# Kernel tuning notes

Hardware: AMD Instinct MI355X
Metric: run time of the kernel (lower is better)

## Reference

```python
import jax, jax.numpy as jnp
import numpy as np

B, L, D = 2, 2048, 2048
H, HKV, HD = 16, 4, 128
GROUPS = H // HKV


def _rope_tables(key):
    # standard RoPE cos/sin tables, shape (B, L, HD)
    inv_freq = 1.0 / (10000.0 ** (jnp.arange(0, HD, 2, dtype=jnp.float32) / HD))
    pos = jnp.arange(L, dtype=jnp.float32)
    freqs = pos[:, None] * inv_freq[None, :]          # (L, HD/2)
    emb = jnp.concatenate([freqs, freqs], axis=-1)    # (L, HD)
    cos = jnp.broadcast_to(jnp.cos(emb)[None], (B, L, HD))
    sin = jnp.broadcast_to(jnp.sin(emb)[None], (B, L, HD))
    return cos, sin


def setup_inputs() -> dict:
    key = jax.random.key(0)
    ks = jax.random.split(key, 5)
    x = jax.random.normal(ks[0], (B, L, D), dtype=jnp.float32)
    cos, sin = _rope_tables(ks[1])
    s = 1.0 / np.sqrt(D)
    Wq = jax.random.normal(ks[2], (D, D), dtype=jnp.float32) * s
    bq = jnp.zeros((D,), dtype=jnp.float32)
    Wkv = jax.random.normal(ks[3], (2 * HKV * HD, D), dtype=jnp.float32) * s
    bkv = jnp.zeros((2 * HKV * HD,), dtype=jnp.float32)
    Wo = jax.random.normal(ks[4], (D, D), dtype=jnp.float32) * s
    bo = jnp.zeros((D,), dtype=jnp.float32)
    return {"x": x, "cos": cos, "sin": sin, "Wq": Wq, "bq": bq,
            "Wkv": Wkv, "bkv": bkv, "Wo": Wo, "bo": bo}


def _rotate_half(t):
    t1, t2 = jnp.split(t, 2, axis=-1)
    return jnp.concatenate([-t2, t1], axis=-1)


def reference(x, cos, sin, Wq, bq, Wkv, bkv, Wo, bo):
    b, l, d = x.shape
    # QKV projections
    q = (x @ Wq.T + bq).reshape(b, l, H, HD)
    kv = (x @ Wkv.T + bkv).reshape(b, l, 2, HKV, HD)
    k, v = kv[:, :, 0], kv[:, :, 1]
    # RoPE (unsqueeze over head dim, layout B,L,H,D)
    c = cos[:, :, None, :]
    s = sin[:, :, None, :]
    q = q * c + _rotate_half(q) * s
    k = k * c + _rotate_half(k) * s
    # GQA: expand kv heads to query heads
    k = jnp.repeat(k, GROUPS, axis=2)
    v = jnp.repeat(v, GROUPS, axis=2)
    # causal attention (flash_attn_func equivalent math)
    scores = jnp.einsum("blhd,bmhd->bhlm", q, k) / jnp.sqrt(jnp.float32(HD))
    mask = jnp.tril(jnp.ones((l, l), dtype=bool))
    scores = jnp.where(mask[None, None], scores, jnp.finfo(scores.dtype).min)
    attn = jax.nn.softmax(scores, axis=-1)
    out = jnp.einsum("bhlm,bmhd->blhd", attn, v).reshape(b, l, H * HD)
    return out @ Wo.T + bo
```

## Files before the change

kernel.cpp:

```cpp
#include <hip/hip_runtime.h>
#include <hip/hip_bf16.h>
#include <cstddef>

constexpr int B = 2, L = 2048, D = 2048;
constexpr int H = 16, HKV = 4, HD = 128;
constexpr int GROUPS = H / HKV;
constexpr int KVD = 2 * HKV * HD;
constexpr int M_ROWS = B * L;
constexpr int QKVW = D + KVD;

typedef __attribute__((ext_vector_type(8))) short short8;
typedef __attribute__((ext_vector_type(4))) short s16x4;
typedef __attribute__((ext_vector_type(4))) float f32x4;

__device__ __forceinline__ short f2bf(float f) {
    union { float f; unsigned u; } v; v.f = f;
    unsigned r = v.u + 0x7FFFu + ((v.u >> 16) & 1u);
    return (short)(r >> 16);
}

__device__ __forceinline__ float fast_exp2(float x) {
#if __has_builtin(__builtin_amdgcn_exp2f)
    return __builtin_amdgcn_exp2f(x);
#else
    return exp2f(x);
#endif
}

__device__ __forceinline__ int invp(int pos) {
    const int b16 = pos >> 4, j = pos & 15;
    return ((b16 >> 1) << 4) + j + ((b16 & 1) << 6);
}

typedef __attribute__((address_space(1))) const void cg_void;
typedef __attribute__((address_space(3))) void lds_void;
__device__ __forceinline__ void gl_lds16(const void* g, void* l) {
    __builtin_amdgcn_global_load_lds((cg_void*)g, (lds_void*)l, 16, 0, 0);
}

__global__ __launch_bounds__(256) void cast_all(
    const float* __restrict__ x, const float* __restrict__ Wq,
    const float* __restrict__ Wkv, const float* __restrict__ Wo,
    const float* __restrict__ bq, const float* __restrict__ bkv,
    short* __restrict__ xb, short* __restrict__ wqkvb, short* __restrict__ wob,
    float* __restrict__ bqkv)
{
    constexpr int n_x   = M_ROWS * D / 4;
    constexpr int n_wq  = D * D / 4;
    constexpr int n_wkv = KVD * D / 4;
    constexpr int n_wo  = D * D / 4;
    constexpr int n_w   = n_x + n_wq + n_wkv + n_wo;
    constexpr int RPW   = D / 4;
    int i = blockIdx.x * 256 + threadIdx.x;
    if (i >= n_w) {
        const int j = i - n_w;
        float4 o;
#pragma unroll
        for (int e = 0; e < 4; ++e) {
            const int idx = j * 4 + e;
            float v;
            if (idx < D)                 v = bq[((idx >> 7) << 7) + invp(idx & 127)];
            else if (idx < D + HKV * HD) v = bkv[(((idx - D) >> 7) << 7) + invp((idx - D) & 127)];
            else                         v = bkv[idx - D];
            (&o.x)[e] = v;
        }
        ((float4*)bqkv)[j] = o;
        return;
    }
    const float* src; short* dst; int isrc;
    if (i < n_x) {
        src = x; dst = xb; isrc = i;
    } else if (i < n_x + n_wq) {
        i -= n_x; src = Wq; dst = wqkvb;
        const int fi = i / RPW, col = i % RPW;
        const int head = fi >> 7, pos = fi & 127;
        isrc = ((head << 7) + invp(pos)) * RPW + col;
    } else if (i < n_x + n_wq + n_wkv) {
        i -= n_x + n_wq; src = Wkv; dst = wqkvb + (size_t)D * D;
        const int fi = i / RPW, col = i % RPW;
        if (fi < HKV * HD) {
            isrc = (((fi >> 7) << 7) + invp(fi & 127)) * RPW + col;
        } else {
            isrc = i;
        }
    } else {
        i -= n_x + n_wq + n_wkv; src = Wo; dst = wob; isrc = i;
    }
    const float4 f = ((const float4*)src)[isrc];
    s16x4 s;
    s[0] = f2bf(f.x); s[1] = f2bf(f.y); s[2] = f2bf(f.z); s[3] = f2bf(f.w);
    ((s16x4*)dst)[i] = s;
}

template<int MODE>
__global__ __launch_bounds__(512, 2) void gemm256(
    const short* __restrict__ Ag, const short* __restrict__ Wg,
    const float* __restrict__ bias, float* __restrict__ C,
    const float* __restrict__ cosp, const float* __restrict__ sinp,
    short* __restrict__ qout, short* __restrict__ kout, short* __restrict__ vtout,
    int M, int N, int K)
{
    __shared__ __align__(1024) char smem[131072];

    const int tid = threadIdx.x;
    const int w = tid >> 6, lane = tid & 63;
    const int quad = lane >> 4, n16 = lane & 15;
    const int wr = w >> 2, wc = w & 3;

    const int nbx = gridDim.x;
    const int nwg = nbx * gridDim.y;
    int wg = blockIdx.y * nbx + blockIdx.x;
    wg = (wg & 7) * (nwg >> 3) + (wg >> 3);
    const int bm = (wg / nbx) << 8;
    const int bn = (wg % nbx) << 8;

    const int nkt = K >> 6;

    const int sbo = n16 * 64 + ((quad * 16) ^ ((n16 & 8) << 2));

    const int srow = lane >> 2;
    const int scol = ((lane & 3) * 8) ^ (((lane >> 5) & 1) << 4);

    f32x4 acc[8][4];
#pragma unroll
    for (int i = 0; i < 8; ++i)
#pragma unroll
        for (int j = 0; j < 4; ++j)
#pragma unroll
            for (int r = 0; r < 4; ++r) acc[i][j][r] = 0.f;

    short8 afr[4][2], bfr[4][2];

#define STAGE_A(k0, cb, h)                                                     \
    { _Pragma("unroll") for (int j = 0; j < 2; ++j) {                          \
        const int s  = w + j * 8;                                              \
        const int u  = s >> 1;                                                 \
        const int rg = ((u >> 2) << 3) + ((h) << 2) + (u & 3);                 \
        const int gr = bm + (rg << 4) + srow;                                  \
        const int gc = (k0) + ((s & 1) << 5) + scol;                           \
        gl_lds16(Ag + (size_t)gr * K + gc,                                     \
                 smem + (cb) * 32768 + (h) * 16384 + (s << 10)); } }

#define STAGE_B(k0, cb, h)                                                     \
    { _Pragma("unroll") for (int j = 0; j < 2; ++j) {                          \
        const int s  = w + j * 8;                                              \
        const int u  = s >> 1;                                                 \
        const int rg = ((u >> 1) << 2) + ((h) << 1) + (u & 1);                 \
        const int gr = bn + (rg << 4) + srow;                                  \
        const int gc = (k0) + ((s & 1) << 5) + scol;                           \
        gl_lds16(Wg + (size_t)gr * K + gc,                                     \
                 smem + 65536 + (cb) * 32768 + (h) * 16384 + (s << 10)); } }

#define PHASE(CB, MH, RDB, STAGE_STMT, WAIT_STMT)                              \
    {                                                                          \
        if (RDB) {                                                             \
            _Pragma("unroll") for (int nj = 0; nj < 4; ++nj)                   \
            _Pragma("unroll") for (int kk = 0; kk < 2; ++kk)                   \
                bfr[nj][kk] = *(const short8*)(smem + 65536 + (CB) * 32768 +   \
                    (nj >> 1) * 16384 +                                        \
                    ((((wc * 2 + (nj & 1)) * 2) + kk) << 10) + sbo);           \
        }                                                                      \
        _Pragma("unroll") for (int mi2 = 0; mi2 < 4; ++mi2)                    \
        _Pragma("unroll") for (int kk = 0; kk < 2; ++kk)                       \
            afr[mi2][kk] = *(const short8*)(smem + (CB) * 32768 +              \
                (MH) * 16384 + ((((wr * 4 + mi2) * 2) + kk) << 10) + sbo);     \
        STAGE_STMT;                                                            \
        WAIT_STMT;                                                             \
        __builtin_amdgcn_s_barrier();                                          \
        asm volatile("s_waitcnt lgkmcnt(0)" ::: "memory");                     \
        __builtin_amdgcn_sched_barrier(0);                                     \
        __builtin_amdgcn_s_setprio(1);                                         \
        _Pragma("unroll") for (int mi2 = 0; mi2 < 4; ++mi2)                    \
        _Pragma("unroll") for (int nj = 0; nj < 4; ++nj)                       \
        _Pragma("unroll") for (int kk = 0; kk < 2; ++kk)                       \
            acc[(MH) * 4 + mi2][nj] =                                          \
                __builtin_amdgcn_mfma_f32_16x16x32_bf16(                       \
                    afr[mi2][kk], bfr[nj][kk], acc[(MH) * 4 + mi2][nj],        \
                    0, 0, 0);                                                  \
        __builtin_amdgcn_s_setprio(0);                                         \
        asm volatile("" ::: "memory");                                         \
        __builtin_amdgcn_s_barrier();                                          \
    }

#define NOP_WAIT asm volatile("" ::: "memory")

    STAGE_A(0, 0, 0);
    STAGE_B(0, 0, 0);
    STAGE_A(0, 0, 1);
    STAGE_B(0, 0, 1);
    if (nkt > 1) {
        STAGE_A(64, 1, 0);
        STAGE_B(64, 1, 0);
        asm volatile("s_waitcnt vmcnt(4)" ::: "memory");
    } else {
        asm volatile("s_waitcnt vmcnt(0)" ::: "memory");
    }
    __builtin_amdgcn_s_barrier();

    for (int t = 0; t < nkt; t += 2) {
        const int k1 = (t + 1) << 6, k2 = (t + 2) << 6, k3 = (t + 3) << 6;
        const bool g2 = (t + 2) < nkt, g3 = (t + 3) < nkt;

        PHASE(0, 0, 1, { STAGE_A(k1, 1, 1); STAGE_B(k1, 1, 1); }, NOP_WAIT);
        PHASE(0, 1, 0, { if (g2) { STAGE_A(k2, 0, 0); STAGE_B(k2, 0, 0); } },
              { if (g2) asm volatile("s_waitcnt vmcnt(4)" ::: "memory");
                else    asm volatile("s_waitcnt vmcnt(0)" ::: "memory"); });

        PHASE(1, 0, 1, { if (g2) { STAGE_A(k2, 0, 1); STAGE_B(k2, 0, 1); } }, NOP_WAIT);
        PHASE(1, 1, 0, { if (g3) { STAGE_A(k3, 1, 0); STAGE_B(k3, 1, 0); } },
              { if (g3) asm volatile("s_waitcnt vmcnt(4)" ::: "memory");
                else    asm volatile("s_waitcnt vmcnt(0)" ::: "memory"); });
    }

#undef PHASE
#undef STAGE_A
#undef STAGE_B
#undef NOP_WAIT

    if (MODE == 0) {
#pragma unroll
        for (int mh = 0; mh < 2; ++mh)
#pragma unroll
            for (int mi2 = 0; mi2 < 4; ++mi2)
#pragma unroll
                for (int r = 0; r < 4; ++r) {
                    const int row = bm + wr * 128 + mh * 64 + mi2 * 16 + quad * 4 + r;
#pragma unroll
                    for (int nh = 0; nh < 2; ++nh)
#pragma unroll
                        for (int ni2 = 0; ni2 < 2; ++ni2) {
                            const int col = bn + wc * 64 + nh * 32 + ni2 * 16 + n16;
                            C[(size_t)row * N + col] =
                                acc[mh * 4 + mi2][nh * 2 + ni2][r] + bias[col];
                        }
                }
    } else {
        short* const T = (short*)smem;
        __syncthreads();
        if (bn < D + HKV * HD) {
#pragma unroll
            for (int mh = 0; mh < 2; ++mh)
#pragma unroll
                for (int mi2 = 0; mi2 < 4; ++mi2)
#pragma unroll
                    for (int r = 0; r < 4; ++r) {
                        const int rl = wr * 128 + mh * 64 + mi2 * 16 + quad * 4 + r;
                        const int row = bm + rl;
                        const float* csrow = cosp + (size_t)row * HD;
                        const float* snrow = sinp + (size_t)row * HD;
                        const int sw = ((rl >> 2) & 7) << 4;
#pragma unroll
                        for (int nh = 0; nh < 2; ++nh) {
                            const int cl = wc * 64 + nh * 32 + n16;
                            const int iif = (wc & 1) * 32 + nh * 16 + n16;
                            const float a  = acc[mh * 4 + mi2][nh * 2 + 0][r] + bias[bn + cl];
                            const float bb = acc[mh * 4 + mi2][nh * 2 + 1][r] + bias[bn + cl + 16];
                            const float olo = a * csrow[iif]       - bb * snrow[iif];
                            const float ohi = bb * csrow[iif + 64] + a * snrow[iif + 64];
                            *(short*)((char*)T + ((rl * 512 + cl * 2) ^ sw))        = f2bf(olo);
                            *(short*)((char*)T + ((rl * 512 + (cl + 16) * 2) ^ sw)) = f2bf(ohi);
                        }
                    }
            __syncthreads();
            const bool isK = (bn >= D);
#pragma unroll
            for (int it = 0; it < 16; ++it) {
                const int idx = it * 512 + tid;
                const int rl = idx >> 5, c8 = idx & 31;
                const short8 v = *(const short8*)((char*)T +
                    ((rl * 512 + c8 * 16) ^ (((rl >> 2) & 7) << 4)));
                const int row = bm + rl;
                if (!isK) {
                    *(short8*)&qout[(size_t)row * D + bn + c8 * 8] = v;
                } else {
                    const int ck = bn - D + c8 * 8;
                    const int hk = ck >> 7, dk = ck & 127;
                    const int b_ = row >> 11, l_ = row & (L - 1);
                    *(short8*)&kout[((size_t)(b_ * HKV + hk) * L + l_) * HD + dk] = v;
                }
            }
        } else {
#pragma unroll
            for (int mh = 0; mh < 2; ++mh)
#pragma unroll
                for (int mi2 = 0; mi2 < 4; ++mi2) {
                    const int l0 = wr * 128 + mh * 64 + mi2 * 16 + quad * 4;
#pragma unroll
                    for (int nh = 0; nh < 2; ++nh)
#pragma unroll
                        for (int ni2 = 0; ni2 < 2; ++ni2) {
                            const int cl = wc * 64 + nh * 32 + ni2 * 16 + n16;
                            const float bs = bias[bn + cl];
                            s16x4 sv;
#pragma unroll
                            for (int r = 0; r < 4; ++r)
                                sv[r] = f2bf(acc[mh * 4 + mi2][nh * 2 + ni2][r] + bs);
                            *(s16x4*)((char*)T + ((cl * 512 + l0 * 2) ^ ((cl & 7) << 4))) = sv;
                        }
                }
            __syncthreads();
#pragma unroll
            for (int it = 0; it < 16; ++it) {
                const int idx = it * 512 + tid;
                const int cvr = idx >> 5, l8 = idx & 31;
                const short8 v = *(const short8*)((char*)T +
                    ((cvr * 512 + l8 * 16) ^ ((cvr & 7) << 4)));
                const int cv = bn - (D + HKV * HD) + cvr;
                const int hv = cv >> 7, dv = cv & 127;
                const int b_ = bm >> 11;
                const int lg = (bm & (L - 1)) + l8 * 8;
                *(short8*)&vtout[((size_t)(b_ * HKV + hv) * HD + dv) * L + lg] = v;
            }
        }
    }
}

__global__ __launch_bounds__(512, 2) void gemm_out(
    const short* __restrict__ Ag, const short* __restrict__ Wg,
    const float* __restrict__ bias, float* __restrict__ C,
    int M, int N, int K)
{
    __shared__ __align__(1024) char smem[98304];

    const int tid = threadIdx.x;
    const int w = tid >> 6, lane = tid & 63;
    const int quad = lane >> 4, n16 = lane & 15;
    const int wr = w >> 2, wc = w & 3;

    const int nbx = gridDim.x;
    const int nwg = nbx * gridDim.y;
    int wg = blockIdx.y * nbx + blockIdx.x;
    wg = (wg & 7) * (nwg >> 3) + (wg >> 3);
    const int bm = (wg / nbx) << 7;
    const int bn = (wg % nbx) << 8;

    const int nkt = K >> 6;

    const int sbo = n16 * 64 + ((quad * 16) ^ ((n16 & 8) << 2));
    const int srow = lane >> 2;
    const int scol = ((lane & 3) * 8) ^ (((lane >> 5) & 1) << 4);

    f32x4 acc[4][4];
#pragma unroll
    for (int i = 0; i < 4; ++i)
#pragma unroll
        for (int j = 0; j < 4; ++j)
#pragma unroll
            for (int r = 0; r < 4; ++r) acc[i][j][r] = 0.f;

    short8 afr[4], bfr[4];

#define OSTAGE_A(k0, cb, kh)                                                   \
    { const int gr = bm + (w << 4) + srow;                                     \
      const int gc = (k0) + ((kh) << 5) + scol;                                \
      gl_lds16(Ag + (size_t)gr * K + gc,                                       \
               smem + (cb) * 16384 + (kh) * 8192 + (w << 10)); }

#define OSTAGE_B(k0, cb, kh)                                                   \
    { _Pragma("unroll") for (int j = 0; j < 2; ++j) {                          \
        const int s = w + j * 8;                                               \
        const int gr = bn + (s << 4) + srow;                                   \
        const int gc = (k0) + ((kh) << 5) + scol;                              \
        gl_lds16(Wg + (size_t)gr * K + gc,                                     \
                 smem + 32768 + (cb) * 32768 + (kh) * 16384 + (s << 10)); } }

#define OPHASE(CB, KH, STAGE_STMT, WAIT_STMT)                                  \
    {                                                                          \
        _Pragma("unroll") for (int mi = 0; mi < 4; ++mi)                       \
            afr[mi] = *(const short8*)(smem + (CB) * 16384 + (KH) * 8192 +     \
                ((wr * 4 + mi) << 10) + sbo);                                  \
        _Pragma("unroll") for (int nj = 0; nj < 4; ++nj)                       \
            bfr[nj] = *(const short8*)(smem + 32768 + (CB) * 32768 +           \
                (KH) * 16384 + ((wc * 4 + nj) << 10) + sbo);                   \
        STAGE_STMT;                                                            \
        WAIT_STMT;                                                             \
        __builtin_amdgcn_s_barrier();                                          \
        asm volatile("s_waitcnt lgkmcnt(0)" ::: "memory");                     \
        __builtin_amdgcn_sched_barrier(0);                                     \
        __builtin_amdgcn_s_setprio(1);                                         \
        _Pragma("unroll") for (int mi = 0; mi < 4; ++mi)                       \
        _Pragma("unroll") for (int nj = 0; nj < 4; ++nj)                       \
            acc[mi][nj] = __builtin_amdgcn_mfma_f32_16x16x32_bf16(             \
                afr[mi], bfr[nj], acc[mi][nj], 0, 0, 0);                       \
        __builtin_amdgcn_s_setprio(0);                                         \
        asm volatile("" ::: "memory");                                         \
        __builtin_amdgcn_s_barrier();                                          \
    }

#define ONOP asm volatile("" ::: "memory")

    OSTAGE_A(0, 0, 0);
    OSTAGE_B(0, 0, 0);
    OSTAGE_A(0, 0, 1);
    OSTAGE_B(0, 0, 1);
    if (nkt > 1) {
        OSTAGE_A(64, 1, 0);
        OSTAGE_B(64, 1, 0);
        asm volatile("s_waitcnt vmcnt(3)" ::: "memory");
    } else {
        asm volatile("s_waitcnt vmcnt(0)" ::: "memory");
    }
    __builtin_amdgcn_s_barrier();

    for (int t = 0; t < nkt; t += 2) {
        const int k1 = (t + 1) << 6, k2 = (t + 2) << 6, k3 = (t + 3) << 6;
        const bool g2 = (t + 2) < nkt, g3 = (t + 3) < nkt;

        OPHASE(0, 0, { OSTAGE_A(k1, 1, 1); OSTAGE_B(k1, 1, 1); }, ONOP);
        OPHASE(0, 1, { if (g2) { OSTAGE_A(k2, 0, 0); OSTAGE_B(k2, 0, 0); } },
               { if (g2) asm volatile("s_waitcnt vmcnt(3)" ::: "memory");
                 else    asm volatile("s_waitcnt vmcnt(0)" ::: "memory"); });

        OPHASE(1, 0, { if (g2) { OSTAGE_A(k2, 0, 1); OSTAGE_B(k2, 0, 1); } }, ONOP);
        OPHASE(1, 1, { if (g3) { OSTAGE_A(k3, 1, 0); OSTAGE_B(k3, 1, 0); } },
               { if (g3) asm volatile("s_waitcnt vmcnt(3)" ::: "memory");
                 else    asm volatile("s_waitcnt vmcnt(0)" ::: "memory"); });
    }

#undef OPHASE
#undef OSTAGE_A
#undef OSTAGE_B
#undef ONOP

#pragma unroll
    for (int mi = 0; mi < 4; ++mi)
#pragma unroll
        for (int r = 0; r < 4; ++r) {
            const int row = bm + wr * 64 + mi * 16 + quad * 4 + r;
#pragma unroll
            for (int nj = 0; nj < 4; ++nj) {
                const int col = bn + wc * 64 + nj * 16 + n16;
                C[(size_t)row * N + col] = acc[mi][nj][r] + bias[col];
            }
        }
}

__global__ __launch_bounds__(512) void attn_mfma4(
    const short* __restrict__ qb_, const short* __restrict__ kb_,
    const short* __restrict__ vtb_, short* __restrict__ ob)
{
    __shared__ __align__(16) char smem[86016];
    short* const KsB  = (short*)smem;
    short* const VtB  = (short*)(smem + 32768);
    short* const PbB  = (short*)(smem + 65536);
    float* const Rbuf = (float*)smem;

    const int hkv = blockIdx.y, b = blockIdx.z;
    const int tid = threadIdx.x;
    const int w = tid >> 6, lane = tid & 63;
    const int quad = lane >> 4, n16 = lane & 15;
    const int h   = hkv * GROUPS + (w & 3);
    const int kh  = (w >> 2) * 32;
    const int khg = (w >> 2) * 4;

    const size_t kbase  = (size_t)(b * HKV + hkv) * L * HD;
    const size_t vtbase = (size_t)(b * HKV + hkv) * HD * L;
    const float c1 = 0.12751845f;
    const float c0 = -28.853901f;

    short8 ones;
#pragma unroll
    for (int i = 0; i < 8; ++i) ones[i] = (short)0x3F80;

    const int kr = lane >> 4;
    const int kg_sw = lane & 15;
    const int vr = lane >> 3;
    const int vg_sw = lane & 7;

    short* const myPb = PbB + w * (2 * 16 * 40);

#pragma unroll 1
    for (int phase = 0; phase < 2; ++phase) {
        const int qidx = phase ? (63 - (int)blockIdx.x) : (int)blockIdx.x;
        const int qb0 = qidx * 32;
        const int ntiles = (qidx >> 1) + 1;

        short8 qf[2][4];
#pragma unroll
        for (int rt = 0; rt < 2; ++rt)
#pragma unroll
            for (int kk = 0; kk < 4; ++kk)
                qf[rt][kk] = *(const short8*)&qb_[
                    ((size_t)(b * L + qb0 + rt * 16 + n16)) * D + h * HD + kk * 32 + quad * 8];

        f32x4 oacc[2][8], lacc[2];
#pragma unroll
        for (int rt = 0; rt < 2; ++rt) {
#pragma unroll
            for (int r = 0; r < 4; ++r) lacc[rt][r] = 0.f;
#pragma unroll
            for (int nt = 0; nt < 8; ++nt)
#pragma unroll
                for (int r = 0; r < 4; ++r) oacc[rt][nt][r] = 0.f;
        }

        __syncthreads();

        {
            const short* kg = kb_ + kbase;
            const short* vg = vtb_ + vtbase;
#pragma unroll
            for (int j = 0; j < 2; ++j) {
                const int chunk = w * 2 + j;
                const int r = chunk * 4 + kr;
                gl_lds16(kg + r * HD + (kg_sw ^ (r & 15)) * 8, KsB + chunk * 512);
            }
#pragma unroll
            for (int j = 0; j < 2; ++j) {
                const int chunk = w * 2 + j;
                const int d = chunk * 8 + vr;
                gl_lds16(vg + (size_t)d * L + (vg_sw ^ (d & 7)) * 8, VtB + chunk * 512);
            }
        }

        for (int kt = 0; kt < ntiles; ++kt) {
            const int buf = kt & 1;
            __syncthreads();

            if (kt + 1 < ntiles) {
                const short* kg = kb_ + kbase + (size_t)((kt + 1) * 64) * HD;
                const short* vg = vtb_ + vtbase + (kt + 1) * 64;
#pragma unroll
                for (int j = 0; j < 2; ++j) {
                    const int chunk = w * 2 + j;
                    const int r = chunk * 4 + kr;
                    gl_lds16(kg + r * HD + (kg_sw ^ (r & 15)) * 8,
                             KsB + (buf ^ 1) * 8192 + chunk * 512);
                }
#pragma unroll
                for (int j = 0; j < 2; ++j) {
                    const int chunk = w * 2 + j;
                    const int d = chunk * 8 + vr;
                    gl_lds16(vg + (size_t)d * L + (vg_sw ^ (d & 7)) * 8,
                             VtB + (buf ^ 1) * 8192 + chunk * 512);
                }
            }

            const short* Ks = KsB + buf * 8192;
            const short* Vt = VtB + buf * 8192;

            f32x4 s[2][2];
#pragma unroll
            for (int rt = 0; rt < 2; ++rt)
#pragma unroll
                for (int ktl = 0; ktl < 2; ++ktl)
#pragma unroll
                    for (int r = 0; r < 4; ++r) s[rt][ktl][r] = 0.f;
            __builtin_amdgcn_s_setprio(1);
#pragma unroll
            for (int kk = 0; kk < 4; ++kk) {
                short8 kf[2];
#pragma unroll
                for (int ktl = 0; ktl < 2; ++ktl) {
                    const int row = kh + ktl * 16 + n16;
                    kf[ktl] = *(const short8*)&Ks[row * 128 + ((kk * 4 + quad) ^ n16) * 8];
                }
#pragma unroll
                for (int rt = 0; rt < 2; ++rt)
#pragma unroll
                    for (int ktl = 0; ktl < 2; ++ktl)
                        s[rt][ktl] = __builtin_amdgcn_mfma_f32_16x16x32_bf16(
                            qf[rt][kk], kf[ktl], s[rt][ktl], 0, 0, 0);
            }
            __builtin_amdgcn_s_setprio(0);

            const bool lastt = (kt == ntiles - 1);
#pragma unroll
            for (int rt = 0; rt < 2; ++rt) {
#pragma unroll
                for (int ktl = 0; ktl < 2; ++ktl) {
                    const int key0 = kt * 64 + kh + ktl * 16 + n16;
#pragma unroll
                    for (int r = 0; r < 4; ++r) {
                        float sv = s[rt][ktl][r];
                        if (lastt) {
                            const int qi = qb0 + rt * 16 + quad * 4 + r;
                            sv = (key0 <= qi) ? sv : -1e30f;
                        }
                        const float e = fast_exp2(sv * c1 + c0);
                        myPb[(rt * 16 + quad * 4 + r) * 40 + ktl * 16 + n16] = f2bf(e);
                    }
                }
            }
            asm volatile("s_waitcnt lgkmcnt(0)" ::: "memory");

            short8 pf[2];
#pragma unroll
            for (int rt = 0; rt < 2; ++rt)
                pf[rt] = *(const short8*)&myPb[(rt * 16 + n16) * 40 + quad * 8];
            __builtin_amdgcn_s_setprio(1);
#pragma unroll
            for (int rt = 0; rt < 2; ++rt)
                lacc[rt] = __builtin_amdgcn_mfma_f32_16x16x32_bf16(pf[rt], ones, lacc[rt], 0, 0, 0);
#pragma unroll
            for (int nt = 0; nt < 8; ++nt) {
                const short8 vf = *(const short8*)&Vt[
                    (nt * 16 + n16) * 64 + ((khg + quad) ^ (n16 & 7)) * 8];
#pragma unroll
                for (int rt = 0; rt < 2; ++rt)
                    oacc[rt][nt] = __builtin_amdgcn_mfma_f32_16x16x32_bf16(pf[rt], vf, oacc[rt][nt], 0, 0, 0);
            }
            __builtin_amdgcn_s_setprio(0);
        }

        __syncthreads();
        if (w >= 4) {
            float* rp = Rbuf + ((size_t)(w - 4) * 64 + lane) * 76;
#pragma unroll
            for (int rt = 0; rt < 2; ++rt)
#pragma unroll
                for (int nt = 0; nt < 8; ++nt)
                    *(f32x4*)&rp[(rt * 8 + nt) * 4] = oacc[rt][nt];
            *(f32x4*)&rp[64] = lacc[0];
            *(f32x4*)&rp[68] = lacc[1];
        }
        __syncthreads();
        if (w < 4) {
            const float* rp = Rbuf + ((size_t)w * 64 + lane) * 76;
#pragma unroll
            for (int rt = 0; rt < 2; ++rt) {
                const f32x4 lr = *(const f32x4*)&rp[64 + rt * 4];
#pragma unroll
                for (int r = 0; r < 4; ++r) lacc[rt][r] += lr[r];
#pragma unroll
                for (int nt = 0; nt < 8; ++nt) {
                    const f32x4 o2 = *(const f32x4*)&rp[(rt * 8 + nt) * 4];
#pragma unroll
                    for (int r = 0; r < 4; ++r) oacc[rt][nt][r] += o2[r];
                }
            }
#pragma unroll
            for (int rt = 0; rt < 2; ++rt) {
#pragma unroll
                for (int r = 0; r < 4; ++r) {
                    const float inv = 1.0f / lacc[rt][r];
                    short* op = ob + ((size_t)(b * L + qb0 + rt * 16 + quad * 4 + r)) * D + h * HD + n16;
#pragma unroll
                    for (int nt = 0; nt < 8; ++nt) op[nt * 16] = f2bf(oacc[rt][nt][r] * inv);
                }
            }
        }
    }
}

extern "C" void kernel_launch(void* const* d_in, const int* in_sizes, int n_in,
                              void* d_out, int out_size, void* d_ws, size_t ws_size,
                              hipStream_t stream)
{
    const float* x    = (const float*)d_in[0];
    const float* cosp = (const float*)d_in[1];
    const float* sinp = (const float*)d_in[2];
    const float* Wq   = (const float*)d_in[3];
    const float* bq   = (const float*)d_in[4];
    const float* Wkv  = (const float*)d_in[5];
    const float* bkv  = (const float*)d_in[6];
    const float* Wo   = (const float*)d_in[7];
    const float* bo   = (const float*)d_in[8];
    float* out = (float*)d_out;

    char* p = (char*)d_ws;
    short* x_bf    = (short*)p; p += (size_t)M_ROWS * D * 2;
    short* wqkv_bf = (short*)p; p += (size_t)QKVW * D * 2;
    short* wo_bf   = (short*)p; p += (size_t)D * D * 2;
    float* b_qkv   = (float*)p; p += (size_t)QKVW * 4;
    short* q_bf    = (short*)p; p += (size_t)M_ROWS * D * 2;
    short* k_bf    = (short*)p; p += (size_t)M_ROWS * HKV * HD * 2;
    short* vt_bf   = (short*)p;
    short* attn_bf = x_bf;

    dim3 blk(256);

    cast_all<<<dim3(18435), blk, 0, stream>>>(
        x, Wq, Wkv, Wo, bq, bkv, x_bf, wqkv_bf, wo_bf, b_qkv);

    gemm256<1><<<dim3(QKVW / 256, M_ROWS / 256), dim3(512), 0, stream>>>(
        x_bf, wqkv_bf, b_qkv, nullptr, cosp, sinp, q_bf, k_bf, vt_bf,
        M_ROWS, QKVW, D);

    attn_mfma4<<<dim3(32, HKV, B), dim3(512), 0, stream>>>(q_bf, k_bf, vt_bf, attn_bf);

    gemm_out<<<dim3(D / 256, M_ROWS / 128), dim3(512), 0, stream>>>(
        attn_bf, wo_bf, bo, out, M_ROWS, D, D);
}
```

Measured before the change: 283.0 us.

## Halve attention query tile to 16 rows and double grid blocks

The attention kernel now processes 16 query rows per block-phase instead of 32. This doubles the grid to 64x4x2 blocks and shrinks the per-wave accumulators, the P staging buffer and the reduction buffer. The aim is more parallelism and occupancy, with launch bounds requesting 4 blocks. In exchange each K/V tile loaded into LDS is reused by half as many query rows, so global and LDS traffic per FLOP rises.

```diff
diff --git a/kernel.cpp b/kernel.cpp
--- a/kernel.cpp
+++ b/kernel.cpp
@@ -435,11 +435,11 @@
         }
 }
 
-__global__ __launch_bounds__(512) void attn_mfma4(
+__global__ __launch_bounds__(512, 4) void attn_mfma5(
     const short* __restrict__ qb_, const short* __restrict__ kb_,
     const short* __restrict__ vtb_, short* __restrict__ ob)
 {
-    __shared__ __align__(16) char smem[86016];
+    __shared__ __align__(16) char smem[75776];
     short* const KsB  = (short*)smem;
     short* const VtB  = (short*)(smem + 32768);
     short* const PbB  = (short*)(smem + 65536);
@@ -467,32 +467,27 @@
     const int vr = lane >> 3;
     const int vg_sw = lane & 7;
 
-    short* const myPb = PbB + w * (2 * 16 * 40);
+    short* const myPb = PbB + w * (16 * 40);
 
 #pragma unroll 1
     for (int phase = 0; phase < 2; ++phase) {
-        const int qidx = phase ? (63 - (int)blockIdx.x) : (int)blockIdx.x;
-        const int qb0 = qidx * 32;
-        const int ntiles = (qidx >> 1) + 1;
-
-        short8 qf[2][4];
-#pragma unroll
-        for (int rt = 0; rt < 2; ++rt)
-#pragma unroll
-            for (int kk = 0; kk < 4; ++kk)
-                qf[rt][kk] = *(const short8*)&qb_[
-                    ((size_t)(b * L + qb0 + rt * 16 + n16)) * D + h * HD + kk * 32 + quad * 8];
-
-        f32x4 oacc[2][8], lacc[2];
-#pragma unroll
-        for (int rt = 0; rt < 2; ++rt) {
-#pragma unroll
-            for (int r = 0; r < 4; ++r) lacc[rt][r] = 0.f;
-#pragma unroll
-            for (int nt = 0; nt < 8; ++nt)
-#pragma unroll
-                for (int r = 0; r < 4; ++r) oacc[rt][nt][r] = 0.f;
-        }
+        const int qidx = phase ? (127 - (int)blockIdx.x) : (int)blockIdx.x;
+        const int qb0 = qidx * 16;
+        const int ntiles = (qidx >> 2) + 1;
+
+        short8 qf[4];
+#pragma unroll
+        for (int kk = 0; kk < 4; ++kk)
+            qf[kk] = *(const short8*)&qb_[
+                ((size_t)(b * L + qb0 + n16)) * D + h * HD + kk * 32 + quad * 8];
+
+        f32x4 oacc[8], lacc;
+#pragma unroll
+        for (int r = 0; r < 4; ++r) lacc[r] = 0.f;
+#pragma unroll
+        for (int nt = 0; nt < 8; ++nt)
+#pragma unroll
+            for (int r = 0; r < 4; ++r) oacc[nt][r] = 0.f;
 
         __syncthreads();
 
@@ -539,13 +534,11 @@
             const short* Ks = KsB + buf * 8192;
             const short* Vt = VtB + buf * 8192;
 
-            f32x4 s[2][2];
-#pragma unroll
-            for (int rt = 0; rt < 2; ++rt)
-#pragma unroll
-                for (int ktl = 0; ktl < 2; ++ktl)
-#pragma unroll
-                    for (int r = 0; r < 4; ++r) s[rt][ktl][r] = 0.f;
+            f32x4 s[2];
+#pragma unroll
+            for (int ktl = 0; ktl < 2; ++ktl)
+#pragma unroll
+                for (int r = 0; r < 4; ++r) s[ktl][r] = 0.f;
             __builtin_amdgcn_s_setprio(1);
 #pragma unroll
             for (int kk = 0; kk < 4; ++kk) {
@@ -556,88 +549,67 @@
                     kf[ktl] = *(const short8*)&Ks[row * 128 + ((kk * 4 + quad) ^ n16) * 8];
                 }
 #pragma unroll
-                for (int rt = 0; rt < 2; ++rt)
-#pragma unroll
-                    for (int ktl = 0; ktl < 2; ++ktl)
-                        s[rt][ktl] = __builtin_amdgcn_mfma_f32_16x16x32_bf16(
-                            qf[rt][kk], kf[ktl], s[rt][ktl], 0, 0, 0);
+                for (int ktl = 0; ktl < 2; ++ktl)
+                    s[ktl] = __builtin_amdgcn_mfma_f32_16x16x32_bf16(
+                        qf[kk], kf[ktl], s[ktl], 0, 0, 0);
             }
             __builtin_amdgcn_s_setprio(0);
 
             const bool lastt = (kt == ntiles - 1);
 #pragma unroll
-            for (int rt = 0; rt < 2; ++rt) {
-#pragma unroll
-                for (int ktl = 0; ktl < 2; ++ktl) {
-                    const int key0 = kt * 64 + kh + ktl * 16 + n16;
-#pragma unroll
-                    for (int r = 0; r < 4; ++r) {
-                        float sv = s[rt][ktl][r];
-                        if (lastt) {
-                            const int qi = qb0 + rt * 16 + quad * 4 + r;
-                            sv = (key0 <= qi) ? sv : -1e30f;
-                        }
-                        const float e = fast_exp2(sv * c1 + c0);
-                        myPb[(rt * 16 + quad * 4 + r) * 40 + ktl * 16 + n16] = f2bf(e);
+            for (int ktl = 0; ktl < 2; ++ktl) {
+                const int key0 = kt * 64 + kh + ktl * 16 + n16;
+#pragma unroll
+                for (int r = 0; r < 4; ++r) {
+                    float sv = s[ktl][r];
+                    if (lastt) {
+                        const int qi = qb0 + quad * 4 + r;
+                        sv = (key0 <= qi) ? sv : -1e30f;
                     }
+                    const float e = fast_exp2(sv * c1 + c0);
+                    myPb[(quad * 4 + r) * 40 + ktl * 16 + n16] = f2bf(e);
                 }
             }
             asm volatile("s_waitcnt lgkmcnt(0)" ::: "memory");
 
-            short8 pf[2];
-#pragma unroll
-            for (int rt = 0; rt < 2; ++rt)
-                pf[rt] = *(const short8*)&myPb[(rt * 16 + n16) * 40 + quad * 8];
+            const short8 pf = *(const short8*)&myPb[n16 * 40 + quad * 8];
             __builtin_amdgcn_s_setprio(1);
-#pragma unroll
-            for (int rt = 0; rt < 2; ++rt)
-                lacc[rt] = __builtin_amdgcn_mfma_f32_16x16x32_bf16(pf[rt], ones, lacc[rt], 0, 0, 0);
+            lacc = __builtin_amdgcn_mfma_f32_16x16x32_bf16(pf, ones, lacc, 0, 0, 0);
 #pragma unroll
             for (int nt = 0; nt < 8; ++nt) {
                 const short8 vf = *(const short8*)&Vt[
                     (nt * 16 + n16) * 64 + ((khg + quad) ^ (n16 & 7)) * 8];
-#pragma unroll
-                for (int rt = 0; rt < 2; ++rt)
-                    oacc[rt][nt] = __builtin_amdgcn_mfma_f32_16x16x32_bf16(pf[rt], vf, oacc[rt][nt], 0, 0, 0);
+                oacc[nt] = __builtin_amdgcn_mfma_f32_16x16x32_bf16(pf, vf, oacc[nt], 0, 0, 0);
             }
             __builtin_amdgcn_s_setprio(0);
         }
 
         __syncthreads();
         if (w >= 4) {
-            float* rp = Rbuf + ((size_t)(w - 4) * 64 + lane) * 76;
-#pragma unroll
-            for (int rt = 0; rt < 2; ++rt)
-#pragma unroll
-                for (int nt = 0; nt < 8; ++nt)
-                    *(f32x4*)&rp[(rt * 8 + nt) * 4] = oacc[rt][nt];
-            *(f32x4*)&rp[64] = lacc[0];
-            *(f32x4*)&rp[68] = lacc[1];
+            float* rp = Rbuf + ((size_t)(w - 4) * 64 + lane) * 40;
+#pragma unroll
+            for (int nt = 0; nt < 8; ++nt)
+                *(f32x4*)&rp[nt * 4] = oacc[nt];
+            *(f32x4*)&rp[32] = lacc;
         }
         __syncthreads();
         if (w < 4) {
-            const float* rp = Rbuf + ((size_t)w * 64 + lane) * 76;
-#pragma unroll
-            for (int rt = 0; rt < 2; ++rt) {
-                const f32x4 lr = *(const f32x4*)&rp[64 + rt * 4];
-#pragma unroll
-                for (int r = 0; r < 4; ++r) lacc[rt][r] += lr[r];
-#pragma unroll
-                for (int nt = 0; nt < 8; ++nt) {
-                    const f32x4 o2 = *(const f32x4*)&rp[(rt * 8 + nt) * 4];
-#pragma unroll
-                    for (int r = 0; r < 4; ++r) oacc[rt][nt][r] += o2[r];
-                }
-            }
-#pragma unroll
-            for (int rt = 0; rt < 2; ++rt) {
-#pragma unroll
-                for (int r = 0; r < 4; ++r) {
-                    const float inv = 1.0f / lacc[rt][r];
-                    short* op = ob + ((size_t)(b * L + qb0 + rt * 16 + quad * 4 + r)) * D + h * HD + n16;
-#pragma unroll
-                    for (int nt = 0; nt < 8; ++nt) op[nt * 16] = f2bf(oacc[rt][nt][r] * inv);
-                }
+            const float* rp = Rbuf + ((size_t)w * 64 + lane) * 40;
+            const f32x4 lr = *(const f32x4*)&rp[32];
+#pragma unroll
+            for (int r = 0; r < 4; ++r) lacc[r] += lr[r];
+#pragma unroll
+            for (int nt = 0; nt < 8; ++nt) {
+                const f32x4 o2 = *(const f32x4*)&rp[nt * 4];
+#pragma unroll
+                for (int r = 0; r < 4; ++r) oacc[nt][r] += o2[r];
+            }
+#pragma unroll
+            for (int r = 0; r < 4; ++r) {
+                const float inv = 1.0f / lacc[r];
+                short* op = ob + ((size_t)(b * L + qb0 + quad * 4 + r)) * D + h * HD + n16;
+#pragma unroll
+                for (int nt = 0; nt < 8; ++nt) op[nt * 16] = f2bf(oacc[nt][r] * inv);
             }
         }
     }
@@ -677,7 +649,7 @@
         x_bf, wqkv_bf, b_qkv, nullptr, cosp, sinp, q_bf, k_bf, vt_bf,
         M_ROWS, QKVW, D);
 
-    attn_mfma4<<<dim3(32, HKV, B), dim3(512), 0, stream>>>(q_bf, k_bf, vt_bf, attn_bf);
+    attn_mfma5<<<dim3(64, HKV, B), dim3(512), 0, stream>>>(q_bf, k_bf, vt_bf, attn_bf);
 
     gemm_out<<<dim3(D / 256, M_ROWS / 128), dim3(512), 0, stream>>>(
         attn_bf, wo_bf, bo, out, M_ROWS, D, D);
```

Measured after the change: 281.5 us. About the same (-0.5%).
